# Kernel optimization log

Measured on AMD Instinct MI355X. Metric: run time of the kernel, lower is better.

The kernel has to match this reference:

```python
import jax, jax.numpy as jnp
import numpy as np

# ---- Config constants (from DGM Config) ----
DIM = 20        # number of assets; inputs have DIM+1 cols (last is time)
DELTA = 0.01    # finite-difference step / covariance scale
RHO = 0.5       # asset correlation
MC = 32         # Config.mc_num
N = 2048        # interior points (inputs holds 2*N rows)
UNITS = 128     # Config.unit_num
LAYERS = 3      # Config.layer_num
SIG = 0.2       # Config._sig
MU = 0.05       # Config._mu
R = 0.05        # Config._r

_cov = DELTA * (np.full((DIM, DIM), RHO, dtype=np.float64) + (1.0 - RHO) * np.eye(DIM))
L_TRIL = jnp.asarray(np.linalg.cholesky(_cov).astype(np.float32))  # (DIM, DIM) lower-tri


def setup_inputs() -> dict:
    key = jax.random.key(0)
    ks = jax.random.split(key, 20)
    d = DIM + 1
    u = lambda k, shp: jax.random.uniform(k, shp, jnp.float32, -0.05, 0.05)
    inp = {
        # strictly positive inputs so boundary prod**(1/DIM) is well-defined
        "inputs": jax.random.uniform(ks[0], (2 * N, d), jnp.float32, 0.1, 1.0),
        "eps": jax.random.normal(ks[1], (MC, N, DIM), jnp.float32),
        "w1": u(ks[2], (d, UNITS)), "b1": u(ks[3], (UNITS,)),
        "uzl": u(ks[4], (d, UNITS)), "wzl": u(ks[5], (UNITS, UNITS)), "bzl": u(ks[6], (UNITS,)),
        "ugl": u(ks[7], (d, UNITS)), "wgl": u(ks[8], (UNITS, UNITS)), "bgl": u(ks[9], (UNITS,)),
        "url": u(ks[10], (d, UNITS)), "wrl": u(ks[11], (UNITS, UNITS)), "brl": u(ks[12], (UNITS,)),
        "uhl": u(ks[13], (d, UNITS)), "whl": u(ks[14], (UNITS, UNITS)), "bhl": u(ks[15], (UNITS,)),
        "w": u(ks[16], (UNITS, 1)), "b": u(ks[17], (1,)),
    }
    return inp


def _value(x, w1, b1, uzl, wzl, bzl, ugl, wgl, bgl, url, wrl, brl, uhl, whl, bhl, w, b):
    # DGM gated residual network; x: (..., DIM+1) -> (..., 1)
    act = jnp.tanh
    s = act(x @ w1 + b1)
    for _ in range(LAYERS):
        z = act(x @ uzl + s @ wzl + bzl)
        g = act(x @ ugl + s @ wgl + bgl)
        r = act(x @ url + s @ wrl + brl)
        h = act(x @ uhl + (s * r) @ whl + bhl)
        s = (1.0 - g) * h + z * s
    return s @ w + b


def reference(inputs, eps, w1, b1, uzl, wzl, bzl, ugl, wgl, bgl, url, wrl, brl,
              uhl, whl, bhl, w, b):
    params = (w1, b1, uzl, wzl, bzl, ugl, wgl, bgl, url, wrl, brl, uhl, whl, bhl, w, b)
    val = lambda x: _value(x, *params)
    x1, x2 = jnp.split(inputs, 2, axis=0)          # interior / boundary points

    # first-order grad of value w.r.t. interior inputs
    fprime = jax.grad(lambda x: val(x).sum())(x1)  # (N, DIM+1)
    drift = jnp.concatenate([MU * x1[:, :-1], jnp.ones((x1.shape[0], 1), x1.dtype)], axis=1)
    term1_1 = jnp.sum(drift * fprime, axis=1)      # (N,)

    # correlated MVN perturbations (reparameterized): loc + eps @ L^T
    loc = x1[:, :-1]                               # (N, DIM)
    sample = loc[None, :, :] + jnp.einsum('mnd,kd->mnk', eps, L_TRIL)  # (MC, N, DIM)
    xdiff = sample * (SIG * loc)[None, :, :]
    violation = jnp.concatenate([xdiff, jnp.zeros((MC, x1.shape[0], 1), x1.dtype)], axis=2)
    xplus = x1[None, :, :] + violation             # (MC, N, DIM+1)

    fprime_plus = jax.grad(lambda x: val(x).sum())(xplus)  # (MC, N, DIM+1)
    term1_2 = jnp.sum(
        jnp.mean((fprime_plus - fprime[None, :, :]) / DELTA * violation, axis=0), axis=1)

    # boundary residual: value - payoff (geometric-mean call payoff)
    payoff = jax.nn.relu(jnp.power(jnp.prod(x2[:, :-1], axis=1), 1.0 / DIM))
    term2 = jnp.squeeze(val(x2), -1) - payoff

    interior = term1_1 + 0.5 * term1_2 - R * jnp.squeeze(val(x1), -1)
    return jnp.concatenate([interior, term2], axis=0)  # (2N,)
```

## Files before the change

### kernel.cpp

```cpp
#include <hip/hip_runtime.h>
#include <math.h>

#define DIMN 20
#define DD 21
#define NN 2048
#define MCN 32
#define UNITS 128
#define SIGC 0.2f
#define MUC 0.05f
#define RC 0.05f
#define DELTAC 0.01f

#define TM 32
#define KCH 16
#define KC3 8
#define PTOT (NN + MCN*NN + NN)
#define NBLK (PTOT/TM)

#define OFF_L 0
#define OFF_WT 512
#define OFF_UZGR (OFF_WT + 4*16384)
#define OFF_WZGR (OFF_UZGR + 8192)
#define OFF_FP1  (OFF_WZGR + 49152)
#define OFF_VAL1 (OFF_FP1 + NN*DD)
#define OFF_VAL2 (OFF_VAL1 + NN)
#define OFF_T12  (OFF_VAL2 + NN)
#define OFF_GATES (OFF_T12 + NN)

#define ST_S1 0
#define ST_Z1 4096
#define ST_G1 8192
#define ST_R1 12288
#define ST_Z2 16384
#define ST_G2 20480
#define ST_R2 24576
#define GB_STRIDE 28672

#define L_TOT_SG 19776
#define L_TOT_RC 23872

#define ELT44(...) _Pragma("unroll") for (int p = 0; p < 4; p++){ _Pragma("unroll") for (int jj = 0; jj < 4; jj++){ __VA_ARGS__; } }

__device__ __forceinline__ int offq(int row, int p0){
    return row*32 + ((p0 + 4*(row&7)) & 31);
}
__device__ __forceinline__ int offs(int row, int p){
    return row*32 + (((p & 28) + 4*(row&7)) & 31) + (p & 3);
}

__device__ __forceinline__ void stageW(const float* __restrict__ g, float* wc, int units){
#if defined(__has_builtin) && __has_builtin(__builtin_amdgcn_global_load_lds)
    int lane = threadIdx.x & 63, wid = threadIdx.x >> 6;
    for (int base = wid*64; base < units; base += 256){
        int u = base + lane;
        if (u < units)
            __builtin_amdgcn_global_load_lds(
                (const __attribute__((address_space(1))) unsigned int*)(g) + (size_t)u*4,
                (__attribute__((address_space(3))) unsigned int*)(wc) + (size_t)base*4,
                16, 0, 0);
    }
#else
    int t = threadIdx.x;
    for (int u = t; u < units; u += 256){
        float4 v = *(const float4*)(g + u*4);
        *(float4*)(wc + u*4) = v;
    }
#endif
}

#define FMA16(acc, s4, w4) \
  acc[0][0]=fmaf(s4.x,w4.x,acc[0][0]); acc[0][1]=fmaf(s4.x,w4.y,acc[0][1]); \
  acc[0][2]=fmaf(s4.x,w4.z,acc[0][2]); acc[0][3]=fmaf(s4.x,w4.w,acc[0][3]); \
  acc[1][0]=fmaf(s4.y,w4.x,acc[1][0]); acc[1][1]=fmaf(s4.y,w4.y,acc[1][1]); \
  acc[1][2]=fmaf(s4.y,w4.z,acc[1][2]); acc[1][3]=fmaf(s4.y,w4.w,acc[1][3]); \
  acc[2][0]=fmaf(s4.z,w4.x,acc[2][0]); acc[2][1]=fmaf(s4.z,w4.y,acc[2][1]); \
  acc[2][2]=fmaf(s4.z,w4.z,acc[2][2]); acc[2][3]=fmaf(s4.z,w4.w,acc[2][3]); \
  acc[3][0]=fmaf(s4.w,w4.x,acc[3][0]); acc[3][1]=fmaf(s4.w,w4.y,acc[3][1]); \
  acc[3][2]=fmaf(s4.w,w4.z,acc[3][2]); acc[3][3]=fmaf(s4.w,w4.w,acc[3][3]);

__device__ __forceinline__ void mm_acc(const float* __restrict__ gW, int K,
    const float* __restrict__ vec, float acc[4][4], float* __restrict__ Wc,
    int jg, int p0)
{
    int nch = (K + KCH - 1) / KCH;
    {
        int r0 = (K < KCH) ? K : KCH;
        stageW(gW, Wc, r0*32);
    }
    for (int c = 0; c < nch; c++){
        __syncthreads();
        if (c + 1 < nch){
            int c0n = (c+1)*KCH;
            int rn = K - c0n; if (rn > KCH) rn = KCH;
            stageW(gW + c0n*UNITS, Wc + ((c+1)&1)*KCH*UNITS, rn*32);
        }
        int c0 = c*KCH;
        int rows = K - c0; if (rows > KCH) rows = KCH;
        const float* wb = Wc + (c&1)*KCH*UNITS;
        if (rows == KCH){
            #pragma unroll
            for (int kk = 0; kk < KCH; kk++){
                int k = c0 + kk;
                float4 w4 = *(const float4*)(wb + kk*UNITS + 4*jg);
                float4 s4 = *(const float4*)(vec + offq(k, p0));
                FMA16(acc, s4, w4)
            }
        } else {
            for (int kk = 0; kk < rows; kk++){
                int k = c0 + kk;
                float4 w4 = *(const float4*)(wb + kk*UNITS + 4*jg);
                float4 s4 = *(const float4*)(vec + offq(k, p0));
                FMA16(acc, s4, w4)
            }
        }
    }
    __syncthreads();
}

__device__ __forceinline__ void mm3_acc(const float* __restrict__ gW, int K,
    const float* __restrict__ vec, float az[4][4], float ag[4][4], float ar[4][4],
    float* __restrict__ Wc, int jg, int p0)
{
    int nch = (K + KC3 - 1) / KC3;
    {
        int r0 = (K < KC3) ? K : KC3;
        stageW(gW, Wc, r0*96);
    }
    for (int c = 0; c < nch; c++){
        __syncthreads();
        if (c + 1 < nch){
            int c0n = (c+1)*KC3;
            int rn = K - c0n; if (rn > KC3) rn = KC3;
            stageW(gW + c0n*384, Wc + ((c+1)&1)*(KC3*384), rn*96);
        }
        int c0 = c*KC3;
        int rows = K - c0; if (rows > KC3) rows = KC3;
        const float* wb = Wc + (c&1)*(KC3*384);
        if (rows == KC3){
            #pragma unroll
            for (int kk = 0; kk < KC3; kk++){
                int k = c0 + kk;
                const float* wrow = wb + kk*384 + 4*jg;
                float4 s4  = *(const float4*)(vec + offq(k, p0));
                float4 wz4 = *(const float4*)(wrow);
                float4 wg4 = *(const float4*)(wrow + 128);
                float4 wr4 = *(const float4*)(wrow + 256);
                FMA16(az, s4, wz4)
                FMA16(ag, s4, wg4)
                FMA16(ar, s4, wr4)
            }
        } else {
            for (int kk = 0; kk < rows; kk++){
                int k = c0 + kk;
                const float* wrow = wb + kk*384 + 4*jg;
                float4 s4  = *(const float4*)(vec + offq(k, p0));
                float4 wz4 = *(const float4*)(wrow);
                float4 wg4 = *(const float4*)(wrow + 128);
                float4 wr4 = *(const float4*)(wrow + 256);
                FMA16(az, s4, wz4)
                FMA16(ag, s4, wg4)
                FMA16(ar, s4, wr4)
            }
        }
    }
    __syncthreads();
}

__device__ __forceinline__ void write_own(float* buf, const float v[4][4], int j0, int p0){
    #pragma unroll
    for (int jj = 0; jj < 4; jj++){
        int j = j0 + jj;
        float4 q = make_float4(v[0][jj], v[1][jj], v[2][jj], v[3][jj]);
        *(float4*)(buf + offq(j, p0)) = q;
    }
}
__device__ __forceinline__ void read_own(const float* buf, float v[4][4], int j0, int p0){
    #pragma unroll
    for (int jj = 0; jj < 4; jj++){
        int j = j0 + jj;
        float4 q = *(const float4*)(buf + offq(j, p0));
        v[0][jj]=q.x; v[1][jj]=q.y; v[2][jj]=q.z; v[3][jj]=q.w;
    }
}
__device__ __forceinline__ void stash_w(float* buf, const float v[4][4], int t){
    #pragma unroll
    for (int jj = 0; jj < 4; jj++)
        *(float4*)(buf + (jj*256 + t)*4) = make_float4(v[0][jj], v[1][jj], v[2][jj], v[3][jj]);
}
__device__ __forceinline__ void stash_r(const float* buf, float v[4][4], int t){
    #pragma unroll
    for (int jj = 0; jj < 4; jj++){
        float4 q = *(const float4*)(buf + (jj*256 + t)*4);
        v[0][jj]=q.x; v[1][jj]=q.y; v[2][jj]=q.z; v[3][jj]=q.w;
    }
}

__device__ __forceinline__ void gate_f(const float* __restrict__ U, const float* __restrict__ W,
    const float* __restrict__ bias, const float* __restrict__ xT, const float* __restrict__ Sin,
    float* __restrict__ Wc, float out[4][4], int jg, int p0, int j0)
{
    float acc[4][4];
    float4 b = *(const float4*)(bias + j0);
    #pragma unroll
    for (int p = 0; p < 4; p++){ acc[p][0]=b.x; acc[p][1]=b.y; acc[p][2]=b.z; acc[p][3]=b.w; }
    mm_acc(U, DD, xT, acc, Wc, jg, p0);
    mm_acc(W, UNITS, Sin, acc, Wc, jg, p0);
    #pragma unroll
    for (int p = 0; p < 4; p++)
        #pragma unroll
        for (int jj = 0; jj < 4; jj++) out[p][jj] = tanhf(acc[p][jj]);
}

__device__ __forceinline__ void gate3_f(const float* __restrict__ Uzgr, const float* __restrict__ Wzgr,
    const float* __restrict__ bz, const float* __restrict__ bg, const float* __restrict__ br,
    const float* __restrict__ xT, const float* __restrict__ Sin,
    float* __restrict__ Wc, float zt[4][4], float gt[4][4], float rt[4][4],
    int jg, int p0, int j0)
{
    float4 b0 = *(const float4*)(bz + j0);
    float4 b1 = *(const float4*)(bg + j0);
    float4 b2 = *(const float4*)(br + j0);
    #pragma unroll
    for (int p = 0; p < 4; p++){
        zt[p][0]=b0.x; zt[p][1]=b0.y; zt[p][2]=b0.z; zt[p][3]=b0.w;
        gt[p][0]=b1.x; gt[p][1]=b1.y; gt[p][2]=b1.z; gt[p][3]=b1.w;
        rt[p][0]=b2.x; rt[p][1]=b2.y; rt[p][2]=b2.z; rt[p][3]=b2.w;
    }
    mm3_acc(Uzgr, DD, xT, zt, gt, rt, Wc, jg, p0);
    mm3_acc(Wzgr, UNITS, Sin, zt, gt, rt, Wc, jg, p0);
    ELT44(zt[p][jj]=tanhf(zt[p][jj]); gt[p][jj]=tanhf(gt[p][jj]); rt[p][jj]=tanhf(rt[p][jj]))
}

__global__ void chol_kernel(float* __restrict__ Lout)
{
    if (threadIdx.x == 0 && blockIdx.x == 0) {
        const double beta = 0.01 * 0.5;
        const double diag = 0.01;
        double c[DIMN], d[DIMN];
        double S = 0.0;
        for (int j = 0; j < DIMN; j++){
            double dj = sqrt(diag - S);
            double cj = (beta - S) / dj;
            d[j] = dj; c[j] = cj;
            S += cj*cj;
        }
        for (int i = 0; i < DIMN; i++)
            for (int j = 0; j < DIMN; j++)
                Lout[i*DIMN + j] = (j < i) ? (float)c[j] : (j == i) ? (float)d[i] : 0.0f;
    }
}

__global__ void transpose_k(const float* __restrict__ wz, const float* __restrict__ wg,
                            const float* __restrict__ wr, const float* __restrict__ wh,
                            float* __restrict__ WT)
{
    int idx = blockIdx.x*256 + threadIdx.x;
    int q = idx >> 14, r2 = idx & 16383, k = r2 >> 7, j = r2 & 127;
    const float* src = (q==0)? wz : (q==1)? wg : (q==2)? wr : wh;
    WT[(q<<14) + j*UNITS + k] = src[k*UNITS + j];
}

__global__ void pack_zgr(const float* __restrict__ uz, const float* __restrict__ ug,
                         const float* __restrict__ ur,
                         const float* __restrict__ wz, const float* __restrict__ wg,
                         const float* __restrict__ wr,
                         float* __restrict__ Uzgr, float* __restrict__ Wzgr)
{
    int idx = blockIdx.x*256 + threadIdx.x;
    if (idx < 128*384){
        int k = idx/384, c = idx - k*384, g = c >> 7, j = c & 127;
        const float* s = (g==0)? wz : (g==1)? wg : wr;
        Wzgr[idx] = s[k*UNITS + j];
        return;
    }
    int i2 = idx - 128*384;
    if (i2 < 21*384){
        int k = i2/384, c = i2 - k*384, g = c >> 7, j = c & 127;
        const float* s = (g==0)? uz : (g==1)? ug : ur;
        Uzgr[i2] = s[k*UNITS + j];
    }
}

#define DGM_PARAMS \
    const float* __restrict__ inputs, const float* __restrict__ eps, \
    const float* __restrict__ w1, const float* __restrict__ b1, \
    const float* __restrict__ uz, const float* __restrict__ bz, \
    const float* __restrict__ ug, const float* __restrict__ bg, \
    const float* __restrict__ ur, const float* __restrict__ br, \
    const float* __restrict__ uh, const float* __restrict__ wh, const float* __restrict__ bh, \
    const float* __restrict__ wv, const float* __restrict__ bv, \
    const float* __restrict__ Lm, const float* __restrict__ WT, \
    const float* __restrict__ Uzgr, const float* __restrict__ Wzgr, \
    float* __restrict__ gws, \
    float* __restrict__ fp1, float* __restrict__ val1, float* __restrict__ val2, \
    float* __restrict__ t12acc

#define DGM_ARGS inputs, eps, w1, b1, uz, bz, ug, bg, ur, br, uh, wh, bh, wv, bv, \
    Lm, WT, Uzgr, Wzgr, gws, fp1, val1, val2, t12acc

template<int SG>
__device__ __forceinline__ void dgm_body(float* lds, DGM_PARAMS)
{
    float* S0 = lds;
    float* S1 = SG ? lds : lds + 4096;
    float* S2 = lds + (SG ? 4096 : 8192);
    float* Db = lds + (SG ? 8192 : 12288);
    float* Wc = lds + (SG ? 12288 : 16384);
    float* xT = lds + (SG ? 18432 : 22528);
    float* Vb = lds + (SG ? 19104 : 23200);

    const int t  = threadIdx.x;
    const int jg = t & 31;
    const int pg = t >> 5;
    const int p0 = pg * 4;
    const int j0 = jg * 4;
    const int P0 = blockIdx.x * TM;
    const int type = (P0 < NN) ? 0 : (P0 < NN + MCN*NN) ? 1 : 2;
    int base_n = 0, mrow = 0;
    if (type == 1){ int q = P0 - NN; mrow = q >> 11; base_n = q & (NN-1); }

    float* gb = gws + (size_t)blockIdx.x * GB_STRIDE;

    {
        int p = t & 31, kq = t >> 5;
        for (int ki = 0; ki < 3; ki++){
            int k = kq + 8*ki;
            if (k > DIMN) break;
            float xv;
            if (type == 0){
                xv = inputs[(P0 + p)*DD + k];
            } else if (type == 2){
                xv = inputs[(NN + (P0 - NN - MCN*NN) + p)*DD + k];
            } else {
                int n = base_n + p;
                float x1v = inputs[n*DD + k];
                if (k == DIMN) xv = x1v;
                else {
                    const float* ep = eps + (size_t)(mrow*NN + n)*DIMN;
                    float a = x1v;
                    for (int d = 0; d < DIMN; d++) a = fmaf(ep[d], Lm[k*DIMN + d], a);
                    float viol = a * (SIGC * x1v);
                    Vb[offs(k, p)] = viol;
                    xv = x1v + viol;
                }
            }
            xT[offs(k, p)] = xv;
        }
    }
    __syncthreads();

    float s_own[4][4];
    {
        float acc[4][4];
        float4 b = *(const float4*)(b1 + j0);
        #pragma unroll
        for (int p = 0; p < 4; p++){ acc[p][0]=b.x; acc[p][1]=b.y; acc[p][2]=b.z; acc[p][3]=b.w; }
        mm_acc(w1, DD, xT, acc, Wc, jg, p0);
        ELT44(s_own[p][jj] = tanhf(acc[p][jj]))
        write_own(S0, s_own, j0, p0);
        __syncthreads();
    }

    float zt[4][4], gt[4][4], rt[4][4], ht[4][4];

#define GATES(SIN, SMUL) \
    gate3_f(Uzgr, Wzgr, bz, bg, br, xT, SIN, Wc, zt, gt, rt, jg, p0, j0); \
    { float tt[4][4]; ELT44(tt[p][jj] = SMUL[p][jj]*rt[p][jj]) write_own(Db, tt, j0, p0); } \
    gate_f(uh, wh, bh, xT, Db, Wc, ht, jg, p0, j0);

#define FWD_LAYER(SIN) \
    GATES(SIN, s_own) \
    ELT44(s_own[p][jj] = (1.f - gt[p][jj])*ht[p][jj] + zt[p][jj]*s_own[p][jj])

    FWD_LAYER(S0)
    if (SG){ if (type != 2){
        stash_w(gb + ST_S1, s_own, t);
        stash_w(gb + ST_Z1, zt, t); stash_w(gb + ST_G1, gt, t); stash_w(gb + ST_R1, rt, t);
    } }
    else   { write_own(S1, s_own, j0, p0); }
    write_own(Db, s_own, j0, p0);

    FWD_LAYER(Db)
    if (SG && type != 2){
        stash_w(gb + ST_Z2, zt, t); stash_w(gb + ST_G2, gt, t); stash_w(gb + ST_R2, rt, t);
    }
    write_own(S2, s_own, j0, p0);

    FWD_LAYER(S2)

    {
        float4 wv4 = *(const float4*)(wv + j0);
        float vs[4];
        #pragma unroll
        for (int p = 0; p < 4; p++)
            vs[p] = s_own[p][0]*wv4.x + s_own[p][1]*wv4.y + s_own[p][2]*wv4.z + s_own[p][3]*wv4.w;
        __syncthreads();
        *(float4*)(Db + jg*32 + p0) = make_float4(vs[0], vs[1], vs[2], vs[3]);
        __syncthreads();
        if (t < TM){
            float v = bv[0];
            for (int j2 = 0; j2 < 32; j2++) v += Db[j2*32 + t];
            if (type == 0) val1[P0 + t] = v;
            else if (type == 2) val2[P0 + t - NN - MCN*NN] = v;
        }
        __syncthreads();
    }
    if (type == 2) return;

    float ds[4][4];
    {
        float4 wv4 = *(const float4*)(wv + j0);
        #pragma unroll
        for (int p = 0; p < 4; p++){ ds[p][0]=wv4.x; ds[p][1]=wv4.y; ds[p][2]=wv4.z; ds[p][3]=wv4.w; }
    }
    float proj[4] = {0.f, 0.f, 0.f, 0.f};
    float dxp[3] = {0.f, 0.f, 0.f};
    const int pi = t >> 3, il = t & 7;

    const float* WTz = WT;
    const float* WTg = WT + 16384;
    const float* WTr = WT + 2*16384;
    const float* WTh = WT + 3*16384;

#define DX_DOT(UMAT) \
    { _Pragma("unroll") for (int ii = 0; ii < 3; ii++){ \
        int i = il + 8*ii; \
        if (i < DD){ \
            const float* Urow = UMAT + i*UNITS; \
            float a = 0.f; \
            for (int j2 = 0; j2 < UNITS; j2++) a = fmaf(Db[offs(j2, pi)], Urow[j2], a); \
            dxp[ii] += a; \
        } } }

#define PROJ_D(UMAT, SEL) \
    { float uv[4][4]; \
      ELT44(uv[p][jj] = 0.f) \
      const float* up_ = UMAT + 4*jg; \
      for (int k = 0; k < DIMN; k++){ \
          float4 w4 = *(const float4*)(up_ + k*UNITS); \
          float4 s4 = *(const float4*)(Vb + offq(k, p0)); \
          FMA16(uv, s4, w4) \
      } \
      ELT44(proj[p] += uv[p][jj]*SEL[p][jj]) }

#define BWD_LAYER(SLP, MODE, GZ, GG, GR) \
    { \
    float dhp[4][4], dgp[4][4], dzp[4][4], dsn[4][4]; \
    { \
    float sl[4][4]; \
    if (MODE == 0){ read_own(S2, sl, j0, p0); } \
    else if (MODE == 2){ stash_r(gb + ST_S1, sl, t); } \
    else { read_own(SLP, sl, j0, p0); } \
    if (MODE == 2 || MODE == 3){ \
        stash_r(gb + GZ, zt, t); stash_r(gb + GG, gt, t); \
        float sn[4][4]; \
        if (MODE == 2){ read_own(S2, sn, j0, p0); } \
        else { stash_r(gb + ST_S1, sn, t); } \
        ELT44(ht[p][jj] = (sn[p][jj] - zt[p][jj]*sl[p][jj]) / (1.f - gt[p][jj])) \
    } \
    if (MODE == 1){ GATES(SLP, sl) } \
    ELT44(float d=ds[p][jj]; float g=gt[p][jj]; float h=ht[p][jj]; \
        dhp[p][jj] = d*(1.f - g)*(1.f - h*h); \
        dgp[p][jj] = -d*h*(1.f - g*g)) \
    ELT44(float d=ds[p][jj]; float z=zt[p][jj]; float s=sl[p][jj]; \
        dzp[p][jj] = d*s*(1.f - z*z); \
        dsn[p][jj] = d*z) \
    } \
    write_own(Db, dhp, j0, p0); \
    if (type == 1){ PROJ_D(uh, dhp) } else { __syncthreads(); DX_DOT(uh) } \
    float dsr[4][4]; \
    ELT44(dsr[p][jj] = 0.f) \
    mm_acc(WTh, UNITS, Db, dsr, Wc, jg, p0); \
    { \
    float rl[4][4], sl2[4][4], drp[4][4]; \
    if (MODE == 2 || MODE == 3){ stash_r(gb + GR, rl, t); } \
    else { ELT44(rl[p][jj] = rt[p][jj]) } \
    if (MODE == 0){ read_own(S2, sl2, j0, p0); } \
    else if (MODE == 2){ stash_r(gb + ST_S1, sl2, t); } \
    else { read_own(SLP, sl2, j0, p0); } \
    ELT44(float dr=dsr[p][jj]; float r=rl[p][jj]; \
        drp[p][jj] = dr*sl2[p][jj]*(1.f - r*r); \
        dsn[p][jj] += dr*r) \
    write_own(Db, dzp, j0, p0); \
    if (type == 1){ PROJ_D(uz, dzp) } else { __syncthreads(); DX_DOT(uz) } \
    mm_acc(WTz, UNITS, Db, dsn, Wc, jg, p0); \
    write_own(Db, dgp, j0, p0); \
    if (type == 1){ PROJ_D(ug, dgp) } else { __syncthreads(); DX_DOT(ug) } \
    mm_acc(WTg, UNITS, Db, dsn, Wc, jg, p0); \
    write_own(Db, drp, j0, p0); \
    if (type == 1){ PROJ_D(ur, drp) } else { __syncthreads(); DX_DOT(ur) } \
    mm_acc(WTr, UNITS, Db, dsn, Wc, jg, p0); \
    } \
    ELT44(ds[p][jj] = dsn[p][jj]) \
    }

    BWD_LAYER(S0, 0, ST_Z2, ST_G2, ST_R2)
    BWD_LAYER(S1, (SG ? 2 : 1), ST_Z2, ST_G2, ST_R2)
    if (SG){ BWD_LAYER(S0, 3, ST_Z1, ST_G1, ST_R1) }
    else   { BWD_LAYER(S0, 1, ST_Z1, ST_G1, ST_R1) }

    {
        float s0l[4][4];
        read_own(S0, s0l, j0, p0);
        float v0[4][4];
        ELT44(v0[p][jj] = ds[p][jj]*(1.f - s0l[p][jj]*s0l[p][jj]))

        if (type == 1){
            PROJ_D(w1, v0)
            __syncthreads();
            *(float4*)(Db + jg*32 + p0) = make_float4(proj[0], proj[1], proj[2], proj[3]);
            __syncthreads();
            if (t < TM){
                float s = 0.f;
                for (int j2 = 0; j2 < 32; j2++) s += Db[j2*32 + t];
                atomicAdd(t12acc + base_n + t, s);
            }
        } else {
            write_own(Db, v0, j0, p0);
            __syncthreads();
            DX_DOT(w1)
            #pragma unroll
            for (int ii = 0; ii < 3; ii++){
                int i = il + 8*ii;
                if (i < DD) fp1[(P0 + pi)*DD + i] = dxp[ii];
            }
        }
    }
}

__global__ __launch_bounds__(256) __attribute__((amdgpu_waves_per_eu(2,2))) void dgm_sg(DGM_PARAMS){
    __shared__ float lds[L_TOT_SG];
    dgm_body<1>(lds, DGM_ARGS);
}
__global__ __launch_bounds__(256) __attribute__((amdgpu_waves_per_eu(2,2))) void dgm_rc(DGM_PARAMS){
    __shared__ float lds[L_TOT_RC];
    dgm_body<0>(lds, DGM_ARGS);
}

__global__ void finalize_k(const float* __restrict__ inputs, const float* __restrict__ eps,
    const float* __restrict__ Lm, const float* __restrict__ fp1, const float* __restrict__ val1,
    const float* __restrict__ val2, const float* __restrict__ t12acc, float* __restrict__ out)
{
    int n = blockIdx.x*256 + threadIdx.x;
    if (n >= NN) return;
    float fp[DD];
    #pragma unroll
    for (int k = 0; k < DD; k++) fp[k] = fp1[n*DD + k];
    float t11 = fp[DIMN];
    #pragma unroll
    for (int k = 0; k < DIMN; k++) t11 = fmaf(MUC*inputs[n*DD + k], fp[k], t11);
    float esum[DIMN];
    #pragma unroll
    for (int d = 0; d < DIMN; d++){
        float a = 0.f;
        for (int m = 0; m < MCN; m++) a += eps[(size_t)(m*NN + n)*DIMN + d];
        esum[d] = a;
    }
    float t12b = 0.f;
    #pragma unroll
    for (int k = 0; k < DIMN; k++){
        float loc = inputs[n*DD + k];
        float ssum = (float)MCN * loc;
        #pragma unroll
        for (int d = 0; d < DIMN; d++) ssum = fmaf(esum[d], Lm[k*DIMN + d], ssum);
        float vsum = ssum * (SIGC*loc);
        t12b = fmaf(fp[k], vsum, t12b);
    }
    float term12 = (t12acc[n] - t12b) * (1.0f/(DELTAC*(float)MCN));
    out[n] = t11 + 0.5f*term12 - RC*val1[n];

    float prod = 1.f;
    #pragma unroll
    for (int k = 0; k < DIMN; k++) prod *= inputs[(NN + n)*DD + k];
    float payoff = powf(prod, 1.0f/(float)DIMN);
    if (!(payoff > 0.f)) payoff = 0.f;
    out[NN + n] = val2[n] - payoff;
}

extern "C" void kernel_launch(void* const* d_in, const int* in_sizes, int n_in,
                              void* d_out, int out_size, void* d_ws, size_t ws_size,
                              hipStream_t stream)
{
    const float* inputs = (const float*)d_in[0];
    const float* eps    = (const float*)d_in[1];
    const float* w1     = (const float*)d_in[2];
    const float* b1     = (const float*)d_in[3];
    const float* uz     = (const float*)d_in[4];
    const float* wz     = (const float*)d_in[5];
    const float* bz     = (const float*)d_in[6];
    const float* ug     = (const float*)d_in[7];
    const float* wg     = (const float*)d_in[8];
    const float* bg     = (const float*)d_in[9];
    const float* urr    = (const float*)d_in[10];
    const float* wr     = (const float*)d_in[11];
    const float* br     = (const float*)d_in[12];
    const float* uh     = (const float*)d_in[13];
    const float* wh     = (const float*)d_in[14];
    const float* bh     = (const float*)d_in[15];
    const float* wv     = (const float*)d_in[16];
    const float* bv     = (const float*)d_in[17];

    float* ws    = (float*)d_ws;
    float* Lm    = ws + OFF_L;
    float* WT    = ws + OFF_WT;
    float* Uzgr  = ws + OFF_UZGR;
    float* Wzgr  = ws + OFF_WZGR;
    float* fp1   = ws + OFF_FP1;
    float* val1  = ws + OFF_VAL1;
    float* val2  = ws + OFF_VAL2;
    float* t12   = ws + OFF_T12;
    float* gates = ws + OFF_GATES;
    float* out   = (float*)d_out;

    hipMemsetAsync(t12, 0, NN*sizeof(float), stream);
    hipLaunchKernelGGL(chol_kernel, dim3(1), dim3(64), 0, stream, Lm);
    hipLaunchKernelGGL(transpose_k, dim3(256), dim3(256), 0, stream, wz, wg, wr, wh, WT);
    hipLaunchKernelGGL(pack_zgr, dim3(224), dim3(256), 0, stream, uz, ug, urr, wz, wg, wr, Uzgr, Wzgr);

    size_t need_bytes = ((size_t)OFF_GATES + (size_t)NBLK * (size_t)GB_STRIDE) * sizeof(float);
    if (ws_size >= need_bytes){
        hipLaunchKernelGGL(dgm_sg, dim3(NBLK), dim3(256), 0, stream,
            inputs, eps, w1, b1, uz, bz, ug, bg, urr, br, uh, wh, bh, wv, bv,
            Lm, WT, Uzgr, Wzgr, gates, fp1, val1, val2, t12);
    } else {
        hipLaunchKernelGGL(dgm_rc, dim3(NBLK), dim3(256), 0, stream,
            inputs, eps, w1, b1, uz, bz, ug, bg, urr, br, uh, wh, bh, wv, bv,
            Lm, WT, Uzgr, Wzgr, gates, fp1, val1, val2, t12);
    }
    hipLaunchKernelGGL(finalize_k, dim3(8), dim3(256), 0, stream,
        inputs, eps, Lm, fp1, val1, val2, t12, out);
}
```

Before: 1.525 ms.

## Reorder backward gate passes and limit unrolling to cut register pressure

Restructures the backward layer so the z and g gate gradients are computed, projected and multiplied one at a time instead of keeping four 4x4 gradient tiles live at once. Gate activations are re-read from the stash or shared memory at each use rather than held across phases. Full unrolls in the weight matmul loops and the projection loop become partial unrolls. The aim is fewer VGPRs, which can raise occupancy or avoid spills, at the cost of extra stash and shared-memory reloads and less instruction-level parallelism.

```diff
diff --git a/kernel.cpp b/kernel.cpp
--- a/kernel.cpp
+++ b/kernel.cpp
@@ -98,7 +98,7 @@
         int rows = K - c0; if (rows > KCH) rows = KCH;
         const float* wb = Wc + (c&1)*KCH*UNITS;
         if (rows == KCH){
-            #pragma unroll
+            #pragma unroll 4
             for (int kk = 0; kk < KCH; kk++){
                 int k = c0 + kk;
                 float4 w4 = *(const float4*)(wb + kk*UNITS + 4*jg);
@@ -137,7 +137,7 @@
         int rows = K - c0; if (rows > KC3) rows = KC3;
         const float* wb = Wc + (c&1)*(KC3*384);
         if (rows == KC3){
-            #pragma unroll
+            #pragma unroll 2
             for (int kk = 0; kk < KC3; kk++){
                 int k = c0 + kk;
                 const float* wrow = wb + kk*384 + 4*jg;
@@ -436,6 +436,7 @@
     { float uv[4][4]; \
       ELT44(uv[p][jj] = 0.f) \
       const float* up_ = UMAT + 4*jg; \
+      _Pragma("unroll 4") \
       for (int k = 0; k < DIMN; k++){ \
           float4 w4 = *(const float4*)(up_ + k*UNITS); \
           float4 s4 = *(const float4*)(Vb + offq(k, p0)); \
@@ -445,52 +446,59 @@
 
 #define BWD_LAYER(SLP, MODE, GZ, GG, GR) \
     { \
-    float dhp[4][4], dgp[4][4], dzp[4][4], dsn[4][4]; \
-    { \
-    float sl[4][4]; \
-    if (MODE == 0){ read_own(S2, sl, j0, p0); } \
-    else if (MODE == 2){ stash_r(gb + ST_S1, sl, t); } \
-    else { read_own(SLP, sl, j0, p0); } \
-    if (MODE == 2 || MODE == 3){ \
-        stash_r(gb + GZ, zt, t); stash_r(gb + GG, gt, t); \
-        float sn[4][4]; \
-        if (MODE == 2){ read_own(S2, sn, j0, p0); } \
-        else { stash_r(gb + ST_S1, sn, t); } \
-        ELT44(ht[p][jj] = (sn[p][jj] - zt[p][jj]*sl[p][jj]) / (1.f - gt[p][jj])) \
+    float dsn[4][4]; \
+    if (MODE == 1){ \
+        float slg[4][4]; read_own(SLP, slg, j0, p0); \
+        GATES(SLP, slg) \
     } \
-    if (MODE == 1){ GATES(SLP, sl) } \
-    ELT44(float d=ds[p][jj]; float g=gt[p][jj]; float h=ht[p][jj]; \
-        dhp[p][jj] = d*(1.f - g)*(1.f - h*h); \
-        dgp[p][jj] = -d*h*(1.f - g*g)) \
-    ELT44(float d=ds[p][jj]; float z=zt[p][jj]; float s=sl[p][jj]; \
-        dzp[p][jj] = d*s*(1.f - z*z); \
-        dsn[p][jj] = d*z) \
+    {  \
+        float sl[4][4], zv[4][4]; \
+        if (MODE == 2){ stash_r(gb + ST_S1, sl, t); stash_r(gb + GZ, zv, t); } \
+        else if (MODE == 3){ read_own(SLP, sl, j0, p0); stash_r(gb + GZ, zv, t); } \
+        else if (MODE == 0){ read_own(S2, sl, j0, p0); ELT44(zv[p][jj] = zt[p][jj]) } \
+        else { read_own(SLP, sl, j0, p0); ELT44(zv[p][jj] = zt[p][jj]) } \
+        float dzp[4][4]; \
+        ELT44(float d=ds[p][jj]; float zz=zv[p][jj]; \
+            dzp[p][jj] = d*sl[p][jj]*(1.f - zz*zz); dsn[p][jj] = d*zz) \
+        write_own(Db, dzp, j0, p0); \
+        if (type == 1){ PROJ_D(uz, dzp) } else { __syncthreads(); DX_DOT(uz) } \
     } \
+    mm_acc(WTz, UNITS, Db, dsn, Wc, jg, p0); \
+    float dhp[4][4]; \
+    {  \
+        float gv[4][4], hv[4][4]; \
+        if (MODE == 2 || MODE == 3){ \
+            float zv[4][4], sl[4][4], sn[4][4]; \
+            stash_r(gb + GZ, zv, t); stash_r(gb + GG, gv, t); \
+            if (MODE == 2){ stash_r(gb + ST_S1, sl, t); read_own(S2, sn, j0, p0); } \
+            else { read_own(SLP, sl, j0, p0); stash_r(gb + ST_S1, sn, t); } \
+            ELT44(hv[p][jj] = (sn[p][jj] - zv[p][jj]*sl[p][jj]) / (1.f - gv[p][jj])) \
+        } else { ELT44(gv[p][jj] = gt[p][jj]; hv[p][jj] = ht[p][jj]) } \
+        float dgp[4][4]; \
+        ELT44(float d=ds[p][jj]; float gg=gv[p][jj]; float hh=hv[p][jj]; \
+            dgp[p][jj] = -d*hh*(1.f - gg*gg); \
+            dhp[p][jj] = d*(1.f - gg)*(1.f - hh*hh)) \
+        write_own(Db, dgp, j0, p0); \
+        if (type == 1){ PROJ_D(ug, dgp) } else { __syncthreads(); DX_DOT(ug) } \
+    } \
+    mm_acc(WTg, UNITS, Db, dsn, Wc, jg, p0); \
     write_own(Db, dhp, j0, p0); \
     if (type == 1){ PROJ_D(uh, dhp) } else { __syncthreads(); DX_DOT(uh) } \
     float dsr[4][4]; \
     ELT44(dsr[p][jj] = 0.f) \
     mm_acc(WTh, UNITS, Db, dsr, Wc, jg, p0); \
-    { \
-    float rl[4][4], sl2[4][4], drp[4][4]; \
-    if (MODE == 2 || MODE == 3){ stash_r(gb + GR, rl, t); } \
-    else { ELT44(rl[p][jj] = rt[p][jj]) } \
-    if (MODE == 0){ read_own(S2, sl2, j0, p0); } \
-    else if (MODE == 2){ stash_r(gb + ST_S1, sl2, t); } \
-    else { read_own(SLP, sl2, j0, p0); } \
-    ELT44(float dr=dsr[p][jj]; float r=rl[p][jj]; \
-        drp[p][jj] = dr*sl2[p][jj]*(1.f - r*r); \
-        dsn[p][jj] += dr*r) \
-    write_own(Db, dzp, j0, p0); \
-    if (type == 1){ PROJ_D(uz, dzp) } else { __syncthreads(); DX_DOT(uz) } \
-    mm_acc(WTz, UNITS, Db, dsn, Wc, jg, p0); \
-    write_own(Db, dgp, j0, p0); \
-    if (type == 1){ PROJ_D(ug, dgp) } else { __syncthreads(); DX_DOT(ug) } \
-    mm_acc(WTg, UNITS, Db, dsn, Wc, jg, p0); \
-    write_own(Db, drp, j0, p0); \
-    if (type == 1){ PROJ_D(ur, drp) } else { __syncthreads(); DX_DOT(ur) } \
+    {  \
+        float rv[4][4], sl[4][4], drp[4][4]; \
+        if (MODE == 2){ stash_r(gb + GR, rv, t); stash_r(gb + ST_S1, sl, t); } \
+        else if (MODE == 3){ stash_r(gb + GR, rv, t); read_own(SLP, sl, j0, p0); } \
+        else if (MODE == 0){ ELT44(rv[p][jj] = rt[p][jj]) read_own(S2, sl, j0, p0); } \
+        else { ELT44(rv[p][jj] = rt[p][jj]) read_own(SLP, sl, j0, p0); } \
+        ELT44(float dr=dsr[p][jj]; float rr=rv[p][jj]; \
+            drp[p][jj] = dr*sl[p][jj]*(1.f - rr*rr); dsn[p][jj] += dr*rr) \
+        write_own(Db, drp, j0, p0); \
+        if (type == 1){ PROJ_D(ur, drp) } else { __syncthreads(); DX_DOT(ur) } \
+    } \
     mm_acc(WTr, UNITS, Db, dsn, Wc, jg, p0); \
-    } \
     ELT44(ds[p][jj] = dsn[p][jj]) \
     }
 
```

Measured after the change: 1.371 ms. -10.1%, faster.
